# Optimization experiments

Hardware: AMD Instinct MI355X
Metric: run time of the kernel (lower is better)

The kernel has to match this reference:

```python
import jax, jax.numpy as jnp
import numpy as np

MIN_DIST = 32  # minimum_extrema_distance from init_kwargs


def _extrema_mask(x):
    # x: [L]. Matches torch: dx padded with 0 on right (>0) and left (<=0);
    # sign = (1 - sign(x)).bool() is True iff x <= 0.
    dx = x[1:] - x[:-1]
    right = jnp.pad(dx, (0, 1)) > 0        # rising on the right
    left = jnp.pad(dx, (1, 0)) <= 0        # non-rising on the left
    neg = x <= 0
    valleys = right & left & neg
    peaks = (~right) & (~left) & (~neg)
    return valleys | peaks


def _suppress(x):
    # Greedy NMS-like suppression over one sample. x: [L]
    L = x.shape[0]
    e = _extrema_mask(x)
    # Sort ALL positions by |x| descending, with non-extrema pushed to the end
    key = jnp.where(e, jnp.abs(x), -jnp.inf)
    order = jnp.argsort(-key)              # candidate j -> original index order[j]
    valid = e[order]                       # which sorted candidates are real extrema
    idx = order                            # original positions, in sorted order

    def step(sec, i):
        # If candidate i not yet suppressed: suppress all candidates within
        # MIN_DIST of its position, then un-suppress itself.
        cond = jnp.logical_not(sec[i])
        window = (idx >= idx[i] - MIN_DIST) & (idx <= idx[i] + MIN_DIST)
        new_sec = jnp.where(cond, (sec | window).at[i].set(False), sec)
        return new_sec, None

    sec0 = jnp.logical_not(valid)          # non-extrema start suppressed
    sec, _ = jax.lax.scan(step, sec0, jnp.arange(L))
    primary_sorted = valid & jnp.logical_not(sec)
    # scatter back to original positions (order is a permutation)
    primary = jnp.zeros((L,), dtype=bool).at[order].set(primary_sorted)
    return jnp.where(primary, x, jnp.zeros_like(x))


def setup_inputs() -> dict:
    key = jax.random.key(0)
    input_ = jax.random.normal(key, (128, 1, 4096), dtype=jnp.float32)
    return {"input_": input_}


def reference(input_):
    x = input_[:, 0, :]                    # [B, L]
    out = jax.vmap(_suppress)(x)           # [B, L]
    return out[:, None, :]                 # [B, 1, L]
```

## Files before the change

### kernel.cpp

```cpp
#include <hip/hip_runtime.h>

#define L 4096
#define NT 256
#define C 16
#define MD 32
#define NC (NT + 4)

typedef unsigned int u32;
typedef unsigned long long u64;

static __device__ __forceinline__ u32 umax(u32 a, u32 b) { return a > b ? a : b; }

__global__ __launch_bounds__(NT) void extrema_nms_kernel(const float* __restrict__ in,
                                                         float* __restrict__ out) {
    __shared__ u32 keyT[NC][C];
    __shared__ u32 winmF[2 * NC];
    __shared__ int flagsF[2];

    const int tid = threadIdx.x;
    const int cc = tid + 2;
    const int base = tid * C;
    const float* xrow = in + (size_t)blockIdx.x * L;

    if (tid < 64) {
        int c = tid >> 4, o = tid & 15;
        int col = (c & 1) + ((c >> 1) ? (NT + 2) : 0);
        keyT[col][o] = 0;
    }
    for (int w = tid; w < 2 * NC; w += NT) winmF[w] = 0;
    if (tid == 0) { flagsF[0] = 0; flagsF[1] = 0; }

    float xv[C];
    #pragma unroll
    for (int k = 0; k < C; k += 4) {
        float4 f = *reinterpret_cast<const float4*>(xrow + base + k);
        xv[k] = f.x; xv[k + 1] = f.y; xv[k + 2] = f.z; xv[k + 3] = f.w;
    }
    float xl = (base > 0) ? xrow[base - 1] : 0.0f;
    float xr = (base + C < L) ? xrow[base + C] : 0.0f;

    u32 key[C];
    #pragma unroll
    for (int o = 0; o < C; ++o) {
        int i = base + o;
        float xi = xv[o];
        float xp = (o == 0) ? xl : xv[o - 1];
        float xn = (o == C - 1) ? xr : xv[o + 1];
        bool right = (i < L - 1) && (xn > xi);
        bool left  = (i == 0) || (xi <= xp);
        bool neg   = (xi <= 0.0f);
        bool ext = (right && left && neg) || (!right && !left && !neg);
        key[o] = ext ? ((__float_as_uint(xi) & 0x7fffffffu) + 1u) : 0u;
    }
    #pragma unroll
    for (int k = 0; k < C; k += 4)
        *reinterpret_cast<uint4*>(&keyT[cc][k]) =
            make_uint4(key[k], key[k + 1], key[k + 2], key[k + 3]);
    u32 run = 0, om = 0;
    #pragma unroll
    for (int o = 0; o < C; ++o) if (key[o] > run) { run = key[o]; om = (u32)o; }

    u32 keptm = 0;
    __syncthreads();

    for (int r = 0; r < 200; ++r) {
        if (r > 0) {
            const int pp = ((r - 1) & 1) * NC;
            int go = flagsF[(r - 1) & 1];
            u32 m0 = winmF[pp + cc - 2], m1 = winmF[pp + cc - 1], m2 = winmF[pp + cc];
            u32 m3 = winmF[pp + cc + 1], m4 = winmF[pp + cc + 2];
            if (!go) break;
            if (tid == 0) flagsF[r & 1] = 0;
            u64 W0 = (u64)(m0 & 0xffffu) | ((u64)(m1 & 0xffffu) << 16)
                   | ((u64)(m2 & 0xffffu) << 32) | ((u64)(m3 & 0xffffu) << 48);
            u32 W1 = m4 & 0xffffu;
            u32 supmask = 0;
            if (W0) { int h0 = 63 - __clzll(W0); supmask = (u32)((2ULL << h0) - 1ULL); }
            if (W1) { int l1 = __ffs(W1) - 1;    supmask |= ~((1u << l1) - 1u); }
            supmask &= 0xffffu;
            if (supmask) {
                #pragma unroll
                for (int o = 0; o < C; ++o) if ((supmask >> o) & 1u) key[o] = 0;
                #pragma unroll
                for (int k = 0; k < C; k += 4)
                    *reinterpret_cast<uint4*>(&keyT[cc][k]) =
                        make_uint4(key[k], key[k + 1], key[k + 2], key[k + 3]);
                run = 0; om = 0;
                #pragma unroll
                for (int o = 0; o < C; ++o) if (key[o] > run) { run = key[o]; om = (u32)o; }
            }
            __syncthreads();
        }
        if (run) {
            uint4 a0 = *reinterpret_cast<const uint4*>(&keyT[cc - 2][0]);
            uint4 a1 = *reinterpret_cast<const uint4*>(&keyT[cc - 2][4]);
            uint4 a2 = *reinterpret_cast<const uint4*>(&keyT[cc - 2][8]);
            uint4 a3 = *reinterpret_cast<const uint4*>(&keyT[cc - 2][12]);
            uint4 b0 = *reinterpret_cast<const uint4*>(&keyT[cc - 1][0]);
            uint4 b1 = *reinterpret_cast<const uint4*>(&keyT[cc - 1][4]);
            uint4 b2 = *reinterpret_cast<const uint4*>(&keyT[cc - 1][8]);
            uint4 b3 = *reinterpret_cast<const uint4*>(&keyT[cc - 1][12]);
            uint4 c0 = *reinterpret_cast<const uint4*>(&keyT[cc + 1][0]);
            uint4 c1 = *reinterpret_cast<const uint4*>(&keyT[cc + 1][4]);
            uint4 c2 = *reinterpret_cast<const uint4*>(&keyT[cc + 1][8]);
            uint4 c3 = *reinterpret_cast<const uint4*>(&keyT[cc + 1][12]);
            uint4 d0 = *reinterpret_cast<const uint4*>(&keyT[cc + 2][0]);
            uint4 d1 = *reinterpret_cast<const uint4*>(&keyT[cc + 2][4]);
            uint4 d2 = *reinterpret_cast<const uint4*>(&keyT[cc + 2][8]);
            uint4 d3 = *reinterpret_cast<const uint4*>(&keyT[cc + 2][12]);
            u32 A[C] = {a0.x,a0.y,a0.z,a0.w, a1.x,a1.y,a1.z,a1.w,
                        a2.x,a2.y,a2.z,a2.w, a3.x,a3.y,a3.z,a3.w};
            u32 B[C] = {b0.x,b0.y,b0.z,b0.w, b1.x,b1.y,b1.z,b1.w,
                        b2.x,b2.y,b2.z,b2.w, b3.x,b3.y,b3.z,b3.w};
            u32 Cc[C] = {c0.x,c0.y,c0.z,c0.w, c1.x,c1.y,c1.z,c1.w,
                         c2.x,c2.y,c2.z,c2.w, c3.x,c3.y,c3.z,c3.w};
            u32 D[C] = {d0.x,d0.y,d0.z,d0.w, d1.x,d1.y,d1.z,d1.w,
                        d2.x,d2.y,d2.z,d2.w, d3.x,d3.y,d3.z,d3.w};
            u32 bL = 0, bR = 0;
            #pragma unroll
            for (int o = 0; o < C; ++o) {
                bL = umax(bL, ((u32)o >= om) ? A[o] : 0u);
                bL = umax(bL, B[o]);
                bR = umax(bR, Cc[o]);
                bR = umax(bR, ((u32)o <= om) ? D[o] : 0u);
            }
            bool win = (bL < run) && (bR <= run);
            u32 wm = win ? (1u << om) : 0u;
            winmF[(r & 1) * NC + cc] = wm;
            if (wm) { keptm |= wm; flagsF[r & 1] = 1; }
        }
        __syncthreads();
    }

    float* orow = out + (size_t)blockIdx.x * L;
    #pragma unroll
    for (int k = 0; k < C; k += 4) {
        float4 f;
        f.x = ((keptm >> (k + 0)) & 1u) ? xv[k + 0] : 0.0f;
        f.y = ((keptm >> (k + 1)) & 1u) ? xv[k + 1] : 0.0f;
        f.z = ((keptm >> (k + 2)) & 1u) ? xv[k + 2] : 0.0f;
        f.w = ((keptm >> (k + 3)) & 1u) ? xv[k + 3] : 0.0f;
        *reinterpret_cast<float4*>(orow + base + k) = f;
    }
}

extern "C" void kernel_launch(void* const* d_in, const int* in_sizes, int n_in,
                              void* d_out, int out_size, void* d_ws, size_t ws_size,
                              hipStream_t stream) {
    const float* in = (const float*)d_in[0];
    float* out = (float*)d_out;
    int rows = in_sizes[0] / L;
    extrema_nms_kernel<<<rows, NT, 0, stream>>>(in, out);
}
```

Measured before the change: 14.05 us.

## Replace neighbor key scans with precomputed prefix/suffix max tables in LDS

Each thread now stores per-chunk prefix-max and suffix-max arrays plus a chunk total in shared memory, laid out column-major. A candidate's left and right competitor maxima then take four scalar LDS reads instead of 64 vector-loaded keys and a 16-step max reduction. The suppression update is moved to the end of each round and rewrites the prefix/suffix tables. This removes most LDS traffic and ALU work per round, at the cost of more LDS writes whenever a chunk changes and a larger shared footprint.

```diff
diff --git a/kernel.cpp b/kernel.cpp
--- a/kernel.cpp
+++ b/kernel.cpp
@@ -3,7 +3,6 @@
 #define L 4096
 #define NT 256
 #define C 16
-#define MD 32
 #define NC (NT + 4)
 
 typedef unsigned int u32;
@@ -13,7 +12,9 @@
 
 __global__ __launch_bounds__(NT) void extrema_nms_kernel(const float* __restrict__ in,
                                                          float* __restrict__ out) {
-    __shared__ u32 keyT[NC][C];
+    __shared__ u32 pfxT[C][NC];
+    __shared__ u32 sfxT[C][NC];
+    __shared__ u32 TA[NC];
     __shared__ u32 winmF[2 * NC];
     __shared__ int flagsF[2];
 
@@ -23,10 +24,12 @@
     const float* xrow = in + (size_t)blockIdx.x * L;
 
     if (tid < 64) {
-        int c = tid >> 4, o = tid & 15;
+        int o = tid >> 2, c = tid & 3;
         int col = (c & 1) + ((c >> 1) ? (NT + 2) : 0);
-        keyT[col][o] = 0;
+        pfxT[o][col] = 0;
+        sfxT[o][col] = 0;
     }
+    if (tid < 2) { TA[tid] = 0; TA[NT + 2 + tid] = 0; }
     for (int w = tid; w < 2 * NC; w += NT) winmF[w] = 0;
     if (tid == 0) { flagsF[0] = 0; flagsF[1] = 0; }
 
@@ -52,82 +55,58 @@
         bool ext = (right && left && neg) || (!right && !left && !neg);
         key[o] = ext ? ((__float_as_uint(xi) & 0x7fffffffu) + 1u) : 0u;
     }
-    #pragma unroll
-    for (int k = 0; k < C; k += 4)
-        *reinterpret_cast<uint4*>(&keyT[cc][k]) =
-            make_uint4(key[k], key[k + 1], key[k + 2], key[k + 3]);
+
     u32 run = 0, om = 0;
-    #pragma unroll
-    for (int o = 0; o < C; ++o) if (key[o] > run) { run = key[o]; om = (u32)o; }
-
+    {
+        u32 p = 0;
+        #pragma unroll
+        for (int o = 0; o < C; ++o) { p = umax(p, key[o]); pfxT[o][cc] = p; }
+        TA[cc] = p;
+        u32 s = 0;
+        #pragma unroll
+        for (int o = C - 1; o >= 0; --o) { s = umax(s, key[o]); sfxT[o][cc] = s; }
+        #pragma unroll
+        for (int o = 0; o < C; ++o) if (key[o] > run) { run = key[o]; om = (u32)o; }
+    }
     u32 keptm = 0;
     __syncthreads();
 
     for (int r = 0; r < 200; ++r) {
-        if (r > 0) {
-            const int pp = ((r - 1) & 1) * NC;
-            int go = flagsF[(r - 1) & 1];
-            u32 m0 = winmF[pp + cc - 2], m1 = winmF[pp + cc - 1], m2 = winmF[pp + cc];
-            u32 m3 = winmF[pp + cc + 1], m4 = winmF[pp + cc + 2];
-            if (!go) break;
-            if (tid == 0) flagsF[r & 1] = 0;
-            u64 W0 = (u64)(m0 & 0xffffu) | ((u64)(m1 & 0xffffu) << 16)
-                   | ((u64)(m2 & 0xffffu) << 32) | ((u64)(m3 & 0xffffu) << 48);
-            u32 W1 = m4 & 0xffffu;
-            u32 supmask = 0;
-            if (W0) { int h0 = 63 - __clzll(W0); supmask = (u32)((2ULL << h0) - 1ULL); }
-            if (W1) { int l1 = __ffs(W1) - 1;    supmask |= ~((1u << l1) - 1u); }
-            supmask &= 0xffffu;
-            if (supmask) {
-                #pragma unroll
-                for (int o = 0; o < C; ++o) if ((supmask >> o) & 1u) key[o] = 0;
-                #pragma unroll
-                for (int k = 0; k < C; k += 4)
-                    *reinterpret_cast<uint4*>(&keyT[cc][k]) =
-                        make_uint4(key[k], key[k + 1], key[k + 2], key[k + 3]);
-                run = 0; om = 0;
-                #pragma unroll
-                for (int o = 0; o < C; ++o) if (key[o] > run) { run = key[o]; om = (u32)o; }
-            }
-            __syncthreads();
-        }
         if (run) {
-            uint4 a0 = *reinterpret_cast<const uint4*>(&keyT[cc - 2][0]);
-            uint4 a1 = *reinterpret_cast<const uint4*>(&keyT[cc - 2][4]);
-            uint4 a2 = *reinterpret_cast<const uint4*>(&keyT[cc - 2][8]);
-            uint4 a3 = *reinterpret_cast<const uint4*>(&keyT[cc - 2][12]);
-            uint4 b0 = *reinterpret_cast<const uint4*>(&keyT[cc - 1][0]);
-            uint4 b1 = *reinterpret_cast<const uint4*>(&keyT[cc - 1][4]);
-            uint4 b2 = *reinterpret_cast<const uint4*>(&keyT[cc - 1][8]);
-            uint4 b3 = *reinterpret_cast<const uint4*>(&keyT[cc - 1][12]);
-            uint4 c0 = *reinterpret_cast<const uint4*>(&keyT[cc + 1][0]);
-            uint4 c1 = *reinterpret_cast<const uint4*>(&keyT[cc + 1][4]);
-            uint4 c2 = *reinterpret_cast<const uint4*>(&keyT[cc + 1][8]);
-            uint4 c3 = *reinterpret_cast<const uint4*>(&keyT[cc + 1][12]);
-            uint4 d0 = *reinterpret_cast<const uint4*>(&keyT[cc + 2][0]);
-            uint4 d1 = *reinterpret_cast<const uint4*>(&keyT[cc + 2][4]);
-            uint4 d2 = *reinterpret_cast<const uint4*>(&keyT[cc + 2][8]);
-            uint4 d3 = *reinterpret_cast<const uint4*>(&keyT[cc + 2][12]);
-            u32 A[C] = {a0.x,a0.y,a0.z,a0.w, a1.x,a1.y,a1.z,a1.w,
-                        a2.x,a2.y,a2.z,a2.w, a3.x,a3.y,a3.z,a3.w};
-            u32 B[C] = {b0.x,b0.y,b0.z,b0.w, b1.x,b1.y,b1.z,b1.w,
-                        b2.x,b2.y,b2.z,b2.w, b3.x,b3.y,b3.z,b3.w};
-            u32 Cc[C] = {c0.x,c0.y,c0.z,c0.w, c1.x,c1.y,c1.z,c1.w,
-                         c2.x,c2.y,c2.z,c2.w, c3.x,c3.y,c3.z,c3.w};
-            u32 D[C] = {d0.x,d0.y,d0.z,d0.w, d1.x,d1.y,d1.z,d1.w,
-                        d2.x,d2.y,d2.z,d2.w, d3.x,d3.y,d3.z,d3.w};
-            u32 bL = 0, bR = 0;
-            #pragma unroll
-            for (int o = 0; o < C; ++o) {
-                bL = umax(bL, ((u32)o >= om) ? A[o] : 0u);
-                bL = umax(bL, B[o]);
-                bR = umax(bR, Cc[o]);
-                bR = umax(bR, ((u32)o <= om) ? D[o] : 0u);
-            }
-            bool win = (bL < run) && (bR <= run);
-            u32 wm = win ? (1u << om) : 0u;
+            u32 bL = umax(sfxT[om][cc - 2], TA[cc - 1]);
+            u32 bR = umax(TA[cc + 1], pfxT[om][cc + 2]);
+            u32 wm = (bL < run && bR <= run) ? (1u << om) : 0u;
             winmF[(r & 1) * NC + cc] = wm;
             if (wm) { keptm |= wm; flagsF[r & 1] = 1; }
+        }
+        __syncthreads();
+
+        int go = flagsF[r & 1];
+        const int pp = (r & 1) * NC;
+        u32 m0 = winmF[pp + cc - 2], m1 = winmF[pp + cc - 1], m2 = winmF[pp + cc];
+        u32 m3 = winmF[pp + cc + 1], m4 = winmF[pp + cc + 2];
+        if (!go) break;
+        if (tid == 0) flagsF[(r + 1) & 1] = 0;
+        u64 W0 = (u64)(m0 & 0xffffu) | ((u64)(m1 & 0xffffu) << 16)
+               | ((u64)(m2 & 0xffffu) << 32) | ((u64)(m3 & 0xffffu) << 48);
+        u32 W1 = m4 & 0xffffu;
+        u32 supmask = 0;
+        if (W0) { int h0 = 63 - __clzll(W0); supmask = (u32)((2ULL << h0) - 1ULL); }
+        if (W1) { int l1 = __ffs(W1) - 1;    supmask |= ~((1u << l1) - 1u); }
+        supmask &= 0xffffu;
+        if (run && supmask) {
+            #pragma unroll
+            for (int o = 0; o < C; ++o) if ((supmask >> o) & 1u) key[o] = 0;
+            u32 p = 0;
+            #pragma unroll
+            for (int o = 0; o < C; ++o) { p = umax(p, key[o]); pfxT[o][cc] = p; }
+            TA[cc] = p;
+            u32 s = 0;
+            #pragma unroll
+            for (int o = C - 1; o >= 0; --o) { s = umax(s, key[o]); sfxT[o][cc] = s; }
+            run = 0; om = 0;
+            #pragma unroll
+            for (int o = 0; o < C; ++o) if (key[o] > run) { run = key[o]; om = (u32)o; }
         }
         __syncthreads();
     }
```

Result: faster. 12.31 us (-12.4%).
